# Kernel optimization log

Measured on AMD Instinct MI355X. Metric: run time of the kernel, lower is better.

Reference implementation:

```python
import jax, jax.numpy as jnp
import numpy as np

B, D3, L, H, O, E, GH = 4096, 288, 32, 512, 96, 8, 128


def _init_linear(key, out_dim, in_dim):
    kw, kb = jax.random.split(key)
    bound = 1.0 / np.sqrt(in_dim)
    W = jax.random.uniform(kw, (out_dim, in_dim), jnp.float32, -bound, bound)
    b = jax.random.uniform(kb, (out_dim,), jnp.float32, -bound, bound)
    return W, b


def setup_inputs() -> dict:
    key = jax.random.key(0)
    ks = jax.random.split(key, 12)
    x = jax.random.normal(ks[0], (B, D3), jnp.float32)
    z = jax.random.normal(ks[1], (B, L), jnp.float32)
    # per-expert weights, stacked on leading expert axis [E, out, in]
    def expert_stack(k, out_dim, in_dim):
        Ws, bs = [], []
        for i in range(E):
            Wi, bi = _init_linear(jax.random.fold_in(k, i), out_dim, in_dim)
            Ws.append(Wi); bs.append(bi)
        return jnp.stack(Ws), jnp.stack(bs)
    W0, b0 = expert_stack(ks[2], H, D3 + L)
    W1, b1 = expert_stack(ks[3], H, H + L)
    W2, b2 = expert_stack(ks[4], H, H + L)
    W3, b3 = expert_stack(ks[5], O, H)
    gW1, gb1 = _init_linear(ks[6], GH, D3 + L)
    gW2, gb2 = _init_linear(ks[7], GH, GH)
    gW3, gb3 = _init_linear(ks[8], E, GH)
    return {"x": x, "z": z, "W0": W0, "b0": b0, "W1": W1, "b1": b1,
            "W2": W2, "b2": b2, "W3": W3, "b3": b3,
            "gW1": gW1, "gb1": gb1, "gW2": gW2, "gb2": gb2,
            "gW3": gW3, "gb3": gb3}


def _gating(x, z, gW1, gb1, gW2, gb2, gW3, gb3):
    h = jnp.concatenate([x, z], axis=1)
    h = jax.nn.elu(h @ gW1.T + gb1)
    h = jax.nn.elu(h @ gW2.T + gb2)
    return jax.nn.softmax(h @ gW3.T + gb3, axis=-1)  # [B, E]


def _blended_linear(g, W, b, h):
    # Original: materializes sum_e g[b,e] * W_e -> [B,out,in], then bmm.
    # Mathematically identical linear form: sum_e g[b,e] * (W_e h_b + b_e).
    return jnp.einsum('be,eoi,bi->bo', g, W, h) + g @ b


def reference(x, z, W0, b0, W1, b1, W2, b2, W3, b3,
              gW1, gb1, gW2, gb2, gW3, gb3):
    g = _gating(x, z, gW1, gb1, gW2, gb2, gW3, gb3)  # [B, E]
    # dropout p=0.0 (eval) -> identity
    h = jax.nn.elu(_blended_linear(g, W0, b0, jnp.concatenate([x, z], axis=1)))
    h = jax.nn.elu(_blended_linear(g, W1, b1, jnp.concatenate([h, z], axis=1)))
    h = jax.nn.elu(_blended_linear(g, W2, b2, jnp.concatenate([h, z], axis=1)))
    out = _blended_linear(g, W3, b3, h)
    return out  # [B, O]
```

## Files before the change

kernel.cpp:

```cpp
#include <hip/hip_runtime.h>
#include <hip/hip_fp16.h>

typedef _Float16 half8 __attribute__((ext_vector_type(8)));
typedef _Float16 half4 __attribute__((ext_vector_type(4)));
typedef float floatx4 __attribute__((ext_vector_type(4)));

__device__ __forceinline__ void async_ld16(const void* g, void* l) {
    __builtin_amdgcn_global_load_lds(
        (const __attribute__((address_space(1))) char*)g,
        (__attribute__((address_space(3))) char*)l, 16, 0, 0);
}

__device__ __forceinline__ float elu_f(float v) {
    return v > 0.f ? v : (__expf(v) - 1.f);
}

__device__ __forceinline__ half4 cvt4(const float* src, int j4) {
    float4 f = ((const float4*)src)[j4];
    half4 h; h.x = (_Float16)f.x; h.y = (_Float16)f.y;
    h.z = (_Float16)f.z; h.w = (_Float16)f.w; return h;
}

__device__ __forceinline__ half8 cvt8(const float* src) {
    float4 f0 = ((const float4*)src)[0];
    float4 f1 = ((const float4*)src)[1];
    half8 h;
    h[0] = (_Float16)f0.x; h[1] = (_Float16)f0.y; h[2] = (_Float16)f0.z; h[3] = (_Float16)f0.w;
    h[4] = (_Float16)f1.x; h[5] = (_Float16)f1.y; h[6] = (_Float16)f1.z; h[7] = (_Float16)f1.w;
    return h;
}

__launch_bounds__(256)
__global__ void gating_conv(const float* __restrict__ x, const float* __restrict__ z,
                            const float* __restrict__ gW1, const float* __restrict__ gW2,
                            const float* __restrict__ gW3,
                            const float* __restrict__ gb1, const float* __restrict__ gb2,
                            const float* __restrict__ gb3,
                            float* __restrict__ g,
                            const float* __restrict__ W0, const float* __restrict__ W1,
                            const float* __restrict__ W2, const float* __restrict__ W3,
                            _Float16* __restrict__ X0,
                            _Float16* __restrict__ h0, _Float16* __restrict__ h1,
                            _Float16* __restrict__ h2,
                            _Float16* __restrict__ Wc0, _Float16* __restrict__ Wc1,
                            _Float16* __restrict__ Wc2, _Float16* __restrict__ Wc3)
{
    __shared__ _Float16 Tbuf[4 * 2 * 16 * 136];

    const int tid = threadIdx.x;

    if (blockIdx.x >= 64) {
        const int S0 = 294912;
        const int S1 = 32768;
        const int S2 = 327680;
        const int S3 = 589824;
        const int S4 = 589824;
        const int S5 = 98304;
        const int S6 = 196608;
        const int TOTAL = S0 + S1 + S2 + S3 + S4 + S5 + S6;
        const int nb = gridDim.x - 64;
        const half4 hz = {};
        for (int i = (blockIdx.x - 64) * blockDim.x + tid; i < TOTAL;
             i += nb * blockDim.x) {
            int j = i;
            if (j < S0) {
                int r = j / 72, c = j - r * 72;
                *(half4*)(X0 + r * 320 + c * 4) = cvt4(x, j);
                continue;
            }
            j -= S0;
            if (j < S1) {
                int r = j / 8, c = j - r * 8;
                *(half4*)(X0 + r * 320 + 288 + c * 4) = cvt4(z, j);
                continue;
            }
            j -= S1;
            if (j < S2) { *(half4*)(Wc0 + j * 4) = cvt4(W0, j); continue; }
            j -= S2;
            if (j < S3) {
                int r = j / 144, c = j - r * 144;
                *(half4*)(Wc1 + r * 576 + c * 4) = (c < 136) ? cvt4(W1, r * 136 + c) : hz;
                continue;
            }
            j -= S3;
            if (j < S4) {
                int r = j / 144, c = j - r * 144;
                *(half4*)(Wc2 + r * 576 + c * 4) = (c < 136) ? cvt4(W2, r * 136 + c) : hz;
                continue;
            }
            j -= S4;
            if (j < S5) { *(half4*)(Wc3 + j * 4) = cvt4(W3, j); continue; }
            j -= S5;
            int buf = j >> 16;
            int r2 = j & 65535;
            int row = r2 >> 4, c = r2 & 15;
            _Float16* h = (buf == 0) ? h0 : ((buf == 1) ? h1 : h2);
            *(half4*)(h + row * 576 + 512 + c * 4) = (c < 8) ? cvt4(z, row * 8 + c) : hz;
        }
        return;
    }

    const int l = tid & 63;
    const int w = tid >> 6;
    const int quad = l >> 4;
    const int mi = l & 15;
    const int kq = quad * 8;
    const int mrow = (blockIdx.x * 4 + w) * 16;

    _Float16* T1 = Tbuf + w * (2 * 16 * 136);
    _Float16* T2 = T1 + 16 * 136;

    floatx4 acc1[8] = {};
    for (int kc = 0; kc < 10; kc++) {
        const int k0 = kc * 32;
        half8 a = (k0 < 288) ? cvt8(x + (size_t)(mrow + mi) * 288 + k0 + kq)
                             : cvt8(z + (size_t)(mrow + mi) * 32 + kq);
#pragma unroll
        for (int t = 0; t < 8; t++) {
            half8 b = cvt8(gW1 + (size_t)(t * 16 + mi) * 320 + k0 + kq);
            acc1[t] = __builtin_amdgcn_mfma_f32_16x16x32_f16(a, b, acc1[t], 0, 0, 0);
        }
    }
#pragma unroll
    for (int t = 0; t < 8; t++) {
        const int n = t * 16 + mi;
        const float bn = gb1[n];
#pragma unroll
        for (int r = 0; r < 4; r++)
            T1[(quad * 4 + r) * 136 + n] = (_Float16)elu_f(acc1[t][r] + bn);
    }

    floatx4 acc2[8] = {};
#pragma unroll
    for (int kc = 0; kc < 4; kc++) {
        const int k0 = kc * 32;
        half8 a = *(const half8*)(T1 + mi * 136 + k0 + kq);
#pragma unroll
        for (int t = 0; t < 8; t++) {
            half8 b = cvt8(gW2 + (size_t)(t * 16 + mi) * 128 + k0 + kq);
            acc2[t] = __builtin_amdgcn_mfma_f32_16x16x32_f16(a, b, acc2[t], 0, 0, 0);
        }
    }
#pragma unroll
    for (int t = 0; t < 8; t++) {
        const int n = t * 16 + mi;
        const float bn = gb2[n];
#pragma unroll
        for (int r = 0; r < 4; r++)
            T2[(quad * 4 + r) * 136 + n] = (_Float16)elu_f(acc2[t][r] + bn);
    }

    floatx4 acc3 = {};
#pragma unroll
    for (int kc = 0; kc < 4; kc++) {
        const int k0 = kc * 32;
        half8 a = *(const half8*)(T2 + mi * 136 + k0 + kq);
        half8 b = (mi < 8) ? cvt8(gW3 + (size_t)mi * 128 + k0 + kq) : half8{};
        acc3 = __builtin_amdgcn_mfma_f32_16x16x32_f16(a, b, acc3, 0, 0, 0);
    }
    const float gb = gb3[mi & 7];
#pragma unroll
    for (int r = 0; r < 4; r++) {
        float logit = acc3[r] + gb;
        float mx = logit;
        mx = fmaxf(mx, __shfl_xor(mx, 1));
        mx = fmaxf(mx, __shfl_xor(mx, 2));
        mx = fmaxf(mx, __shfl_xor(mx, 4));
        float e = __expf(logit - mx);
        float s = e;
        s += __shfl_xor(s, 1);
        s += __shfl_xor(s, 2);
        s += __shfl_xor(s, 4);
        if (mi < 8)
            g[(size_t)(mrow + quad * 4 + r) * 8 + mi] = e / s;
    }
}

template <bool ELU_ACT, typename OUT_T>
__launch_bounds__(256, 4)
__global__ void blend64(const _Float16* __restrict__ A, int lda,
                        const _Float16* __restrict__ W, int ldw,
                        int Hdim, int K,
                        const float* __restrict__ g,
                        const float* __restrict__ bias,
                        OUT_T* __restrict__ out, int ldo)
{
    __shared__ __align__(16) char smem_raw[32768];
    _Float16* sA = (_Float16*)smem_raw;
    _Float16* sB = (_Float16*)(smem_raw + 16384);
    float* sredf = (float*)smem_raw;
    __shared__ float sg[128][9];
    __shared__ float sbias[8][16];

    const int tid = threadIdx.x;
    const int l = tid & 63;
    const int w = tid >> 6;
    const int wm = w >> 1, wn = w & 1;
    const int o0 = blockIdx.x * 16;
    const int m0 = blockIdx.y * 128;

    for (int t = tid; t < 128 * 8; t += 256)
        sg[t >> 3][t & 7] = g[(size_t)(m0 + (t >> 3)) * 8 + (t & 7)];
    for (int t = tid; t < 128; t += 256)
        sbias[t >> 4][t & 15] = bias[(t >> 4) * Hdim + o0 + (t & 15)];

    const int lr = l >> 3;
    const int lc = l & 7;
    const int swz = lc ^ lr;

    const _Float16* gAp = A + (size_t)(m0 + w * 64 + lr) * lda + swz * 8;
    _Float16* lAp = sA + w * 4096;
    const int wb = w - 2;
    const int eb = wb * 4;
    const _Float16* gBe = W + ((size_t)eb * Hdim + o0 + lr) * ldw + swz * 8;
    const _Float16* gBo = gBe + (size_t)8 * ldw;
    _Float16* lBp = sB + wb * 4096;

    const int mi = l & 15, quad = l >> 4;
    const int cswz = mi & 7;
    const int offh0 = ((quad ^ cswz) * 8);
    const int offh1 = (((quad + 4) ^ cswz) * 8);
    const _Float16* rAb = sA + (wm * 64 + mi) * 64;
    const _Float16* rBb = sB + (wn * 64 + mi) * 64;

    floatx4 acc[4][4] = {};

    for (int k0 = 0; k0 < K; k0 += 64) {
        __syncthreads();
        if (w < 2) {
            const _Float16* gp = gAp + k0;
            _Float16* lp = lAp;
#pragma unroll
            for (int c = 0; c < 8; c++) {
                async_ld16(gp, lp);
                gp += (size_t)8 * lda;
                lp += 512;
            }
        } else {
            const _Float16* ge = gBe + k0;
            const _Float16* go = gBo + k0;
            _Float16* lp = lBp;
#pragma unroll
            for (int c2 = 0; c2 < 4; c2++) {
                async_ld16(ge, lp); lp += 512;
                async_ld16(go, lp); lp += 512;
                ge += (size_t)Hdim * ldw;
                go += (size_t)Hdim * ldw;
            }
        }
        __syncthreads();
#pragma unroll
        for (int h = 0; h < 2; h++) {
            const int off = h ? offh1 : offh0;
            half8 af[4], bf[4];
#pragma unroll
            for (int i = 0; i < 4; i++) af[i] = *(const half8*)(rAb + i * 1024 + off);
#pragma unroll
            for (int j = 0; j < 4; j++) bf[j] = *(const half8*)(rBb + j * 1024 + off);
#pragma unroll
            for (int i = 0; i < 4; i++)
#pragma unroll
                for (int j = 0; j < 4; j++)
                    acc[i][j] = __builtin_amdgcn_mfma_f32_16x16x32_f16(af[i], bf[j], acc[i][j], 0, 0, 0);
        }
    }

    float p[4][4];
#pragma unroll
    for (int i = 0; i < 4; i++)
#pragma unroll
        for (int r = 0; r < 4; r++) {
            int mloc = wm * 64 + i * 16 + quad * 4 + r;
            float s = 0.f;
#pragma unroll
            for (int j = 0; j < 4; j++) {
                int e = wn * 4 + j;
                s += sg[mloc][e] * (acc[i][j][r] + sbias[e][mi]);
            }
            p[i][r] = s;
        }

    __syncthreads();
    if (wn == 0) {
#pragma unroll
        for (int i = 0; i < 4; i++)
#pragma unroll
            for (int r = 0; r < 4; r++)
                sredf[(wm * 64 + i * 16 + quad * 4 + r) * 17 + mi] = p[i][r];
    }
    __syncthreads();
    if (wn == 1) {
#pragma unroll
        for (int i = 0; i < 4; i++)
#pragma unroll
            for (int r = 0; r < 4; r++) {
                int mrel = i * 16 + quad * 4 + r;
                float v = p[i][r] + sredf[(wm * 64 + mrel) * 17 + mi];
                if (ELU_ACT) v = elu_f(v);
                out[(size_t)(m0 + wm * 64 + mrel) * ldo + o0 + mi] = (OUT_T)v;
            }
    }
}

extern "C" void kernel_launch(void* const* d_in, const int* in_sizes, int n_in,
                              void* d_out, int out_size, void* d_ws, size_t ws_size,
                              hipStream_t stream)
{
    (void)in_sizes; (void)n_in; (void)out_size; (void)ws_size;
    const float* x   = (const float*)d_in[0];
    const float* z   = (const float*)d_in[1];
    const float* W0  = (const float*)d_in[2];
    const float* b0  = (const float*)d_in[3];
    const float* W1  = (const float*)d_in[4];
    const float* b1  = (const float*)d_in[5];
    const float* W2  = (const float*)d_in[6];
    const float* b2  = (const float*)d_in[7];
    const float* W3  = (const float*)d_in[8];
    const float* b3  = (const float*)d_in[9];
    const float* gW1 = (const float*)d_in[10];
    const float* gb1 = (const float*)d_in[11];
    const float* gW2 = (const float*)d_in[12];
    const float* gb2 = (const float*)d_in[13];
    const float* gW3 = (const float*)d_in[14];
    const float* gb3 = (const float*)d_in[15];

    char* p = (char*)d_ws;
    auto alloc = [&](size_t n) { char* r = p; p += (n + 255) & ~(size_t)255; return r; };
    _Float16* X0   = (_Float16*)alloc((size_t)4096 * 320 * 2);
    _Float16* h0   = (_Float16*)alloc((size_t)4096 * 576 * 2);
    _Float16* h1   = (_Float16*)alloc((size_t)4096 * 576 * 2);
    _Float16* h2   = (_Float16*)alloc((size_t)4096 * 576 * 2);
    _Float16* Wc0  = (_Float16*)alloc((size_t)8 * 512 * 320 * 2);
    _Float16* Wc1  = (_Float16*)alloc((size_t)8 * 512 * 576 * 2);
    _Float16* Wc2  = (_Float16*)alloc((size_t)8 * 512 * 576 * 2);
    _Float16* Wc3  = (_Float16*)alloc((size_t)8 * 96 * 512 * 2);
    float*    g    = (float*)alloc((size_t)4096 * 8 * 4);

    gating_conv<<<1024, 256, 0, stream>>>(x, z, gW1, gW2, gW3, gb1, gb2, gb3, g,
                                          W0, W1, W2, W3, X0, h0, h1, h2,
                                          Wc0, Wc1, Wc2, Wc3);

    blend64<true, _Float16><<<dim3(32, 32), 256, 0, stream>>>(X0, 320, Wc0, 320, 512, 320, g, b0, h0, 576);
    blend64<true, _Float16><<<dim3(32, 32), 256, 0, stream>>>(h0, 576, Wc1, 576, 512, 576, g, b1, h1, 576);
    blend64<true, _Float16><<<dim3(32, 32), 256, 0, stream>>>(h1, 576, Wc2, 576, 512, 576, g, b2, h2, 576);
    blend64<false, float><<<dim3(6, 32), 256, 0, stream>>>(h2, 576, Wc3, 512, 96, 512, g, b3, (float*)d_out, 96);
}
```

Baseline: 223.7 us.

## Split gating from conversion kernel and feed it pre-converted fp16 operands

The fused kernel that ran gating on 64 blocks alongside the fp32-to-fp16 conversion is split in two. A conversion kernel now also converts the gating weights, and a separate gating kernel reads fp16 X0 and weights directly, prefetches the next A fragment, and reuses one LDS tile for both hidden layers. This removes repeated fp32 loads and conversions in the gating path. The cost is an extra kernel launch and a serial dependency, since gating now waits for the whole conversion instead of overlapping with it.

Measured after the change: 192.8 us. 13.8% less time.

```diff
diff --git a/kernel.cpp b/kernel.cpp
--- a/kernel.cpp
+++ b/kernel.cpp
@@ -21,85 +21,93 @@
     h.z = (_Float16)f.z; h.w = (_Float16)f.w; return h;
 }
 
-__device__ __forceinline__ half8 cvt8(const float* src) {
-    float4 f0 = ((const float4*)src)[0];
-    float4 f1 = ((const float4*)src)[1];
-    half8 h;
-    h[0] = (_Float16)f0.x; h[1] = (_Float16)f0.y; h[2] = (_Float16)f0.z; h[3] = (_Float16)f0.w;
-    h[4] = (_Float16)f1.x; h[5] = (_Float16)f1.y; h[6] = (_Float16)f1.z; h[7] = (_Float16)f1.w;
-    return h;
-}
-
 __launch_bounds__(256)
-__global__ void gating_conv(const float* __restrict__ x, const float* __restrict__ z,
+__global__ void convert_all(const float* __restrict__ x, const float* __restrict__ z,
+                            const float* __restrict__ W0, const float* __restrict__ W1,
+                            const float* __restrict__ W2, const float* __restrict__ W3,
                             const float* __restrict__ gW1, const float* __restrict__ gW2,
                             const float* __restrict__ gW3,
-                            const float* __restrict__ gb1, const float* __restrict__ gb2,
-                            const float* __restrict__ gb3,
-                            float* __restrict__ g,
-                            const float* __restrict__ W0, const float* __restrict__ W1,
-                            const float* __restrict__ W2, const float* __restrict__ W3,
                             _Float16* __restrict__ X0,
                             _Float16* __restrict__ h0, _Float16* __restrict__ h1,
                             _Float16* __restrict__ h2,
                             _Float16* __restrict__ Wc0, _Float16* __restrict__ Wc1,
-                            _Float16* __restrict__ Wc2, _Float16* __restrict__ Wc3)
+                            _Float16* __restrict__ Wc2, _Float16* __restrict__ Wc3,
+                            _Float16* __restrict__ gW1c, _Float16* __restrict__ gW2c,
+                            _Float16* __restrict__ gW3c)
 {
-    __shared__ _Float16 Tbuf[4 * 2 * 16 * 136];
-
-    const int tid = threadIdx.x;
-
-    if (blockIdx.x >= 64) {
-        const int S0 = 294912;
-        const int S1 = 32768;
-        const int S2 = 327680;
-        const int S3 = 589824;
-        const int S4 = 589824;
-        const int S5 = 98304;
-        const int S6 = 196608;
-        const int TOTAL = S0 + S1 + S2 + S3 + S4 + S5 + S6;
-        const int nb = gridDim.x - 64;
-        const half4 hz = {};
-        for (int i = (blockIdx.x - 64) * blockDim.x + tid; i < TOTAL;
-             i += nb * blockDim.x) {
-            int j = i;
-            if (j < S0) {
-                int r = j / 72, c = j - r * 72;
-                *(half4*)(X0 + r * 320 + c * 4) = cvt4(x, j);
-                continue;
-            }
-            j -= S0;
-            if (j < S1) {
-                int r = j / 8, c = j - r * 8;
-                *(half4*)(X0 + r * 320 + 288 + c * 4) = cvt4(z, j);
-                continue;
-            }
-            j -= S1;
-            if (j < S2) { *(half4*)(Wc0 + j * 4) = cvt4(W0, j); continue; }
-            j -= S2;
-            if (j < S3) {
-                int r = j / 144, c = j - r * 144;
-                *(half4*)(Wc1 + r * 576 + c * 4) = (c < 136) ? cvt4(W1, r * 136 + c) : hz;
-                continue;
-            }
-            j -= S3;
-            if (j < S4) {
-                int r = j / 144, c = j - r * 144;
-                *(half4*)(Wc2 + r * 576 + c * 4) = (c < 136) ? cvt4(W2, r * 136 + c) : hz;
-                continue;
-            }
-            j -= S4;
-            if (j < S5) { *(half4*)(Wc3 + j * 4) = cvt4(W3, j); continue; }
-            j -= S5;
+    const int S0 = 294912;
+    const int S1 = 32768;
+    const int S2 = 327680;
+    const int S3 = 589824;
+    const int S4 = 589824;
+    const int S5 = 98304;
+    const int S6 = 196608;
+    const int S7 = 10240;
+    const int S8 = 4096;
+    const int TOTAL = S0 + S1 + S2 + S3 + S4 + S5 + S6 + S7 + S8 + 256;
+    const half4 hz = {};
+
+    for (int i = blockIdx.x * blockDim.x + threadIdx.x; i < TOTAL;
+         i += gridDim.x * blockDim.x) {
+        int j = i;
+        if (j < S0) {
+            int r = j / 72, c = j - r * 72;
+            *(half4*)(X0 + r * 320 + c * 4) = cvt4(x, j);
+            continue;
+        }
+        j -= S0;
+        if (j < S1) {
+            int r = j / 8, c = j - r * 8;
+            *(half4*)(X0 + r * 320 + 288 + c * 4) = cvt4(z, j);
+            continue;
+        }
+        j -= S1;
+        if (j < S2) { *(half4*)(Wc0 + j * 4) = cvt4(W0, j); continue; }
+        j -= S2;
+        if (j < S3) {
+            int r = j / 144, c = j - r * 144;
+            *(half4*)(Wc1 + r * 576 + c * 4) = (c < 136) ? cvt4(W1, r * 136 + c) : hz;
+            continue;
+        }
+        j -= S3;
+        if (j < S4) {
+            int r = j / 144, c = j - r * 144;
+            *(half4*)(Wc2 + r * 576 + c * 4) = (c < 136) ? cvt4(W2, r * 136 + c) : hz;
+            continue;
+        }
+        j -= S4;
+        if (j < S5) { *(half4*)(Wc3 + j * 4) = cvt4(W3, j); continue; }
+        j -= S5;
+        if (j < S6) {
             int buf = j >> 16;
             int r2 = j & 65535;
             int row = r2 >> 4, c = r2 & 15;
             _Float16* h = (buf == 0) ? h0 : ((buf == 1) ? h1 : h2);
             *(half4*)(h + row * 576 + 512 + c * 4) = (c < 8) ? cvt4(z, row * 8 + c) : hz;
-        }
-        return;
-    }
-
+            continue;
+        }
+        j -= S6;
+        if (j < S7) { *(half4*)(gW1c + j * 4) = cvt4(gW1, j); continue; }
+        j -= S7;
+        if (j < S8) { *(half4*)(gW2c + j * 4) = cvt4(gW2, j); continue; }
+        j -= S8;
+        *(half4*)(gW3c + j * 4) = cvt4(gW3, j);
+    }
+}
+
+__launch_bounds__(256)
+__global__ void gating_fast(const _Float16* __restrict__ X0,
+                            const _Float16* __restrict__ gW1c,
+                            const _Float16* __restrict__ gW2c,
+                            const _Float16* __restrict__ gW3c,
+                            const float* __restrict__ gb1,
+                            const float* __restrict__ gb2,
+                            const float* __restrict__ gb3,
+                            float* __restrict__ g)
+{
+    __shared__ _Float16 Tbuf[4 * 16 * 136];
+
+    const int tid = threadIdx.x;
     const int l = tid & 63;
     const int w = tid >> 6;
     const int quad = l >> 4;
@@ -107,17 +115,19 @@
     const int kq = quad * 8;
     const int mrow = (blockIdx.x * 4 + w) * 16;
 
-    _Float16* T1 = Tbuf + w * (2 * 16 * 136);
-    _Float16* T2 = T1 + 16 * 136;
+    _Float16* T = Tbuf + w * (16 * 136);
+    const _Float16* arow = X0 + (size_t)(mrow + mi) * 320;
 
     floatx4 acc1[8] = {};
+    half8 a_nxt = *(const half8*)(arow + kq);
+#pragma unroll
     for (int kc = 0; kc < 10; kc++) {
         const int k0 = kc * 32;
-        half8 a = (k0 < 288) ? cvt8(x + (size_t)(mrow + mi) * 288 + k0 + kq)
-                             : cvt8(z + (size_t)(mrow + mi) * 32 + kq);
+        half8 a = a_nxt;
+        if (kc < 9) a_nxt = *(const half8*)(arow + k0 + 32 + kq);
 #pragma unroll
         for (int t = 0; t < 8; t++) {
-            half8 b = cvt8(gW1 + (size_t)(t * 16 + mi) * 320 + k0 + kq);
+            half8 b = *(const half8*)(gW1c + (size_t)(t * 16 + mi) * 320 + k0 + kq);
             acc1[t] = __builtin_amdgcn_mfma_f32_16x16x32_f16(a, b, acc1[t], 0, 0, 0);
         }
     }
@@ -127,17 +137,17 @@
         const float bn = gb1[n];
 #pragma unroll
         for (int r = 0; r < 4; r++)
-            T1[(quad * 4 + r) * 136 + n] = (_Float16)elu_f(acc1[t][r] + bn);
+            T[(quad * 4 + r) * 136 + n] = (_Float16)elu_f(acc1[t][r] + bn);
     }
 
     floatx4 acc2[8] = {};
 #pragma unroll
     for (int kc = 0; kc < 4; kc++) {
         const int k0 = kc * 32;
-        half8 a = *(const half8*)(T1 + mi * 136 + k0 + kq);
+        half8 a = *(const half8*)(T + mi * 136 + k0 + kq);
 #pragma unroll
         for (int t = 0; t < 8; t++) {
-            half8 b = cvt8(gW2 + (size_t)(t * 16 + mi) * 128 + k0 + kq);
+            half8 b = *(const half8*)(gW2c + (size_t)(t * 16 + mi) * 128 + k0 + kq);
             acc2[t] = __builtin_amdgcn_mfma_f32_16x16x32_f16(a, b, acc2[t], 0, 0, 0);
         }
     }
@@ -147,15 +157,15 @@
         const float bn = gb2[n];
 #pragma unroll
         for (int r = 0; r < 4; r++)
-            T2[(quad * 4 + r) * 136 + n] = (_Float16)elu_f(acc2[t][r] + bn);
+            T[(quad * 4 + r) * 136 + n] = (_Float16)elu_f(acc2[t][r] + bn);
     }
 
     floatx4 acc3 = {};
 #pragma unroll
     for (int kc = 0; kc < 4; kc++) {
         const int k0 = kc * 32;
-        half8 a = *(const half8*)(T2 + mi * 136 + k0 + kq);
-        half8 b = (mi < 8) ? cvt8(gW3 + (size_t)mi * 128 + k0 + kq) : half8{};
+        half8 a = *(const half8*)(T + mi * 136 + k0 + kq);
+        half8 b = (mi < 8) ? *(const half8*)(gW3c + (size_t)mi * 128 + k0 + kq) : half8{};
         acc3 = __builtin_amdgcn_mfma_f32_16x16x32_f16(a, b, acc3, 0, 0, 0);
     }
     const float gb = gb3[mi & 7];
@@ -334,11 +344,16 @@
     _Float16* Wc1  = (_Float16*)alloc((size_t)8 * 512 * 576 * 2);
     _Float16* Wc2  = (_Float16*)alloc((size_t)8 * 512 * 576 * 2);
     _Float16* Wc3  = (_Float16*)alloc((size_t)8 * 96 * 512 * 2);
+    _Float16* gW1c = (_Float16*)alloc((size_t)128 * 320 * 2);
+    _Float16* gW2c = (_Float16*)alloc((size_t)128 * 128 * 2);
+    _Float16* gW3c = (_Float16*)alloc((size_t)8 * 128 * 2);
     float*    g    = (float*)alloc((size_t)4096 * 8 * 4);
 
-    gating_conv<<<1024, 256, 0, stream>>>(x, z, gW1, gW2, gW3, gb1, gb2, gb3, g,
-                                          W0, W1, W2, W3, X0, h0, h1, h2,
-                                          Wc0, Wc1, Wc2, Wc3);
+    convert_all<<<1024, 256, 0, stream>>>(x, z, W0, W1, W2, W3, gW1, gW2, gW3,
+                                          X0, h0, h1, h2, Wc0, Wc1, Wc2, Wc3,
+                                          gW1c, gW2c, gW3c);
+
+    gating_fast<<<64, 256, 0, stream>>>(X0, gW1c, gW2c, gW3c, gb1, gb2, gb3, g);
 
     blend64<true, _Float16><<<dim3(32, 32), 256, 0, stream>>>(X0, 320, Wc0, 320, 512, 320, g, b0, h0, 576);
     blend64<true, _Float16><<<dim3(32, 32), 256, 0, stream>>>(h0, 576, Wc1, 576, 512, 576, g, b1, h1, 576);
```
